# Optimization experiments

Hardware: AMD Instinct MI355X
Metric: run time of the kernel (lower is better)

## Reference

```python
import jax, jax.numpy as jnp
import numpy as np
from jax import lax

B, N, S, NSAMPLE = 8, 4096, 1024, 32
RADIUS = 0.2
EPS = 1e-5
IN_CH = 64
MLP = [64, 64, 128]


def _fps(xyz, npoint):
    # farthest point sampling; deterministic start at index 0 (torch uses a random start)
    b, n, _ = xyz.shape
    bidx = jnp.arange(b)

    def step(carry, _):
        distance, farthest = carry
        centroid = xyz[bidx, farthest][:, None, :]            # [B,1,3]
        d = jnp.sum((xyz - centroid) ** 2, axis=-1)           # [B,N]
        distance = jnp.minimum(distance, d)
        nxt = jnp.argmax(distance, axis=-1).astype(jnp.int32)
        return (distance, nxt), farthest

    init = (jnp.full((b, n), 1e10, dtype=xyz.dtype), jnp.zeros((b,), jnp.int32))
    _, idxs = lax.scan(step, init, None, length=npoint)
    return idxs.T                                             # [B,npoint]


def _index_points(p, idx):
    # p: [B,N,C], idx: [B,...] -> [B,...,C]
    return jax.vmap(lambda pp, ii: pp[ii])(p, idx)


def _square_distance(src, dst):
    # src [B,S,3], dst [B,N,3] -> [B,S,N]
    d = -2.0 * jnp.einsum('bsc,bnc->bsn', src, dst)
    d += jnp.sum(src ** 2, -1)[:, :, None]
    d += jnp.sum(dst ** 2, -1)[:, None, :]
    return d


def _query_ball(radius, nsample, xyz, new_xyz):
    n = xyz.shape[1]
    sqr = _square_distance(new_xyz, xyz)                      # [B,S,N]
    gidx = jnp.where(sqr > radius ** 2, n, jnp.arange(n, dtype=jnp.int32))
    gidx = jnp.sort(gidx, axis=-1)[:, :, :nsample]            # [B,S,nsample]
    first = gidx[:, :, :1]
    return jnp.where(gidx == n, first, gidx)


def setup_inputs() -> dict:
    key = jax.random.key(0)
    ks = jax.random.split(key, 8)
    inp = {
        'xyz': jax.random.uniform(ks[0], (B, N, 3), jnp.float32),
        'points': jax.random.normal(ks[1], (B, N, IN_CH), jnp.float32),
    }
    last = IN_CH + 3
    for i, out_c in enumerate(MLP):
        scale = 1.0 / np.sqrt(last)
        inp[f'w{i}'] = jax.random.normal(ks[2 + i], (out_c, last), jnp.float32) * scale
        inp[f'b{i}'] = jnp.zeros((out_c,), jnp.float32)
        inp[f'g{i}'] = jnp.ones((out_c,), jnp.float32)
        inp[f'be{i}'] = jnp.zeros((out_c,), jnp.float32)
        last = out_c
    return inp


def _forward(xyz, points, params):
    fps_idx = _fps(xyz, S)
    new_xyz = _index_points(xyz, fps_idx)                     # [B,S,3]
    idx = _query_ball(RADIUS, NSAMPLE, xyz, new_xyz)          # [B,S,n]
    grouped_xyz = _index_points(xyz, idx) - new_xyz[:, :, None, :]
    h = jnp.concatenate([grouped_xyz, _index_points(points, idx)], axis=-1)  # [B,S,n,67]
    for (w, b, g, be) in params:
        h = jnp.einsum('bsnc,oc->bsno', h, w) + b             # 1x1 conv
        mu = jnp.mean(h, axis=(0, 1, 2))
        var = jnp.var(h, axis=(0, 1, 2))                      # training-mode batch norm
        h = jax.nn.relu((h - mu) * lax.rsqrt(var + EPS) * g + be)
    new_points = jnp.max(h, axis=2)                           # [B,S,Cout]
    return new_xyz, jnp.transpose(new_points, (0, 2, 1))      # [B,Cout,S] like torch


def reference(xyz, points, w0, b0, g0, be0, w1, b1, g1, be1, w2, b2, g2, be2):
    params = [(w0, b0, g0, be0), (w1, b1, g1, be1), (w2, b2, g2, be2)]
    return _forward(xyz, points, params)
```

## Files before the change

### kernel.cpp

```cpp
#include <hip/hip_runtime.h>
#include <stdint.h>

#define NB 8
#define NPTS 4096
#define NS 1024
#define NK 32
#define NROWS (NB*NS*NK)
#define R2 0.04f
#define NCOPY 8

typedef __attribute__((ext_vector_type(8))) short bf16x8;
typedef __attribute__((ext_vector_type(4))) float f32x4;

__device__ __forceinline__ float bf2f(uint16_t u){
    uint32_t v = ((uint32_t)u) << 16;
    return __uint_as_float(v);
}
__device__ __forceinline__ uint16_t f2bf(float f){
    uint32_t u = __float_as_uint(f);
    uint32_t r = (u + 0x7FFFu + ((u >> 16) & 1u)) >> 16;
    return (uint16_t)r;
}
__device__ __forceinline__ bf16x8 load_bf8(const uint16_t* p){
    return *reinterpret_cast<const bf16x8*>(p);
}

#define DPPMAX64(key, ctrl, rmask)                                             \
    {                                                                          \
        uint32_t _lo = (uint32_t)(key), _hi = (uint32_t)((key) >> 32);         \
        uint32_t _olo = (uint32_t)__builtin_amdgcn_update_dpp(                 \
            0, (int)_lo, (ctrl), (rmask), 0xf, true);                          \
        uint32_t _ohi = (uint32_t)__builtin_amdgcn_update_dpp(                 \
            0, (int)_hi, (ctrl), (rmask), 0xf, true);                          \
        unsigned long long _o = (((unsigned long long)_ohi) << 32) | _olo;     \
        key = (_o > (key)) ? _o : (key);                                       \
    }

#define FT 16
__global__ __launch_bounds__(256) void fps_kernel(const float* __restrict__ xyz,
                                                  float* __restrict__ out_newxyz){
    __shared__ float LX[NPTS], LY[NPTS], LZ[NPTS];
    __shared__ float4 SC[NS];
    __shared__ unsigned long long cand[2][4];
    const int b = blockIdx.x, t = threadIdx.x;
    const float* base = xyz + (size_t)b * (NPTS*3);
    float px[FT], py[FT], pz[FT], pd[FT];
#pragma unroll
    for (int j = 0; j < FT; ++j){
        int i = t*FT + j;
        float x = base[i*3+0], y = base[i*3+1], z = base[i*3+2];
        px[j]=x; py[j]=y; pz[j]=z; pd[j]=1e10f;
        LX[i]=x; LY[i]=y; LZ[i]=z;
    }
    __syncthreads();
    int cur = 0;
    const int wave = t >> 6, lane = t & 63;
    for (int s = 0; s < NS; ++s){
        float cx = LX[cur], cy = LY[cur], cz = LZ[cur];
        if (t == 0) SC[s] = make_float4(cx, cy, cz, 0.f);
        float bestd = -1.0f; int besti = 0;
#pragma unroll
        for (int j = 0; j < FT; ++j){
            float d;
            {
#pragma clang fp contract(off)
                float dx = px[j]-cx, dy = py[j]-cy, dz = pz[j]-cz;
                d = ((dx*dx) + (dy*dy)) + (dz*dz);
            }
            float nd = fminf(pd[j], d);
            pd[j] = nd;
            if (nd > bestd){ bestd = nd; besti = t*FT + j; }
        }
        unsigned long long key =
            (((unsigned long long)__float_as_uint(bestd)) << 32) |
            (unsigned long long)(~(unsigned)besti);
        DPPMAX64(key, 0x111, 0xf);
        DPPMAX64(key, 0x112, 0xf);
        DPPMAX64(key, 0x114, 0xf);
        DPPMAX64(key, 0x118, 0xf);
        DPPMAX64(key, 0x142, 0xa);
        DPPMAX64(key, 0x143, 0xc);
        int p = s & 1;
        if (lane == 63) cand[p][wave] = key;
        __syncthreads();
        unsigned long long k0 = cand[p][0], k1 = cand[p][1];
        unsigned long long k2 = cand[p][2], k3 = cand[p][3];
        unsigned long long m01 = (k0 > k1) ? k0 : k1;
        unsigned long long m23 = (k2 > k3) ? k2 : k3;
        unsigned long long km  = (m01 > m23) ? m01 : m23;
        cur = (int)(~(uint32_t)km);
    }
    __syncthreads();
    for (int i = t; i < NS; i += 256){
        float4 c = SC[i];
        float* o = out_newxyz + ((size_t)b*NS + i)*3;
        o[0] = c.x; o[1] = c.y; o[2] = c.z;
    }
}

__global__ __launch_bounds__(256) void qball_kernel(const float* __restrict__ xyz,
                                                    const float* __restrict__ newxyz,
                                                    int* __restrict__ idx_out){
    int gid = blockIdx.x*256 + threadIdx.x;
    int w = gid >> 6, lane = gid & 63;
    int b = w >> 10;
    const float* q = newxyz + (size_t)w*3;
    float qx = q[0], qy = q[1], qz = q[2];
    float qn = qx*qx;
    qn = fmaf(qy, qy, qn);
    qn = fmaf(qz, qz, qn);
    const float* base = xyz + (size_t)b * (NPTS*3);
    int cnt = 0, first = 0;
    for (int c0 = 0; c0 < NPTS; c0 += 64){
        int i = c0 + lane;
        float x = base[i*3+0], y = base[i*3+1], z = base[i*3+2];
        float xn = x*x;
        xn = fmaf(y, y, xn);
        xn = fmaf(z, z, xn);
        float dot = qx*x;
        dot = fmaf(qy, y, dot);
        dot = fmaf(qz, z, dot);
        float d;
        {
#pragma clang fp contract(off)
            d = -2.0f * dot;
            d = d + qn;
            d = d + xn;
        }
        bool in = !(d > R2);
        unsigned long long m = __ballot(in);
        if (in){
            int rank = __popcll(m & ((1ull << lane) - 1ull));
            int pos = cnt + rank;
            if (pos < NK) idx_out[(size_t)w*NK + pos] = i;
        }
        if (cnt == 0 && m) first = c0 + (__ffsll((unsigned long long)m) - 1);
        cnt += __popcll(m);
        if (cnt >= NK) break;
    }
    if (cnt < NK){
        for (int p = cnt + lane; p < NK; p += 64) idx_out[(size_t)w*NK + p] = first;
    }
}

__global__ void prep_kernel(const float* __restrict__ w0, const float* __restrict__ w1,
                            const float* __restrict__ w2, uint16_t* __restrict__ w0b,
                            uint16_t* __restrict__ w1b, uint16_t* __restrict__ w2b){
    int t = blockIdx.x*256 + threadIdx.x;
    int stride = gridDim.x*256;
    for (int i = t; i < 64*96; i += stride){
        int n = i/96, c = i%96;
        w0b[i] = (c < 67) ? f2bf(w0[n*67 + c]) : (uint16_t)0;
    }
    for (int i = t; i < 64*64; i += stride)  w1b[i] = f2bf(w1[i]);
    for (int i = t; i < 128*64; i += stride) w2b[i] = f2bf(w2[i]);
}

__global__ __launch_bounds__(256) void layer0_mfma(const float* __restrict__ xyz,
                                                   const float* __restrict__ pts,
                                                   const int* __restrict__ idx,
                                                   const float* __restrict__ newxyz,
                                                   const uint16_t* __restrict__ w0b,
                                                   const float* __restrict__ b0,
                                                   uint16_t* __restrict__ z0,
                                                   double* __restrict__ accumOut){
    __shared__ float S_s[16][64], S_q[16][64];
    const int wave = threadIdx.x >> 6, lane = threadIdx.x & 63;
    const int q = lane >> 4, l16 = lane & 15;
    const int r0 = blockIdx.x*64 + wave*16;
    const int row = r0 + l16;
    const int b = row >> 15;
    const int bs = row >> 5;
    const int id = idx[row];
    const float* prow = pts + (((size_t)b << 12) + id)*64;
    const float* xr   = xyz + (((size_t)b << 12) + id)*3;
    const float* qr   = newxyz + (size_t)bs*3;
    float d0 = xr[0]-qr[0], d1 = xr[1]-qr[1], d2 = xr[2]-qr[2];

    bf16x8 Bf[4][3];
#pragma unroll
    for (int nt = 0; nt < 4; ++nt)
#pragma unroll
        for (int s = 0; s < 3; ++s)
            Bf[nt][s] = load_bf8(w0b + (nt*16 + l16)*96 + s*32 + q*8);

    f32x4 acc[4];
#pragma unroll
    for (int nt = 0; nt < 4; ++nt) acc[nt] = (f32x4){0.f,0.f,0.f,0.f};

#pragma unroll
    for (int s = 0; s < 3; ++s){
        const int k0 = s*32 + q*8;
        bf16x8 a;
#pragma unroll
        for (int j = 0; j < 8; ++j){
            int k = k0 + j;
            float v = (k < 3) ? ((k == 0) ? d0 : ((k == 1) ? d1 : d2))
                              : ((k < 67) ? prow[k-3] : 0.f);
            a[j] = (short)f2bf(v);
        }
#pragma unroll
        for (int nt = 0; nt < 4; ++nt)
            acc[nt] = __builtin_amdgcn_mfma_f32_16x16x32_bf16(a, Bf[nt][s], acc[nt], 0, 0, 0);
    }
#pragma unroll
    for (int nt = 0; nt < 4; ++nt){
        int c = nt*16 + l16;
        float bb = b0[c];
        float sps = 0.f, spq = 0.f;
#pragma unroll
        for (int reg = 0; reg < 4; ++reg){
            int rr = r0 + q*4 + reg;
            float h = acc[nt][reg] + bb;
            sps += h;
            spq = fmaf(h, h, spq);
            z0[(size_t)rr*64 + c] = f2bf(h);
        }
        S_s[wave*4 + q][c] = sps;
        S_q[wave*4 + q][c] = spq;
    }
    __syncthreads();
    int t = threadIdx.x;
    if (t < 64){
        double ss = 0.0, sq = 0.0;
#pragma unroll
        for (int i = 0; i < 16; ++i){ ss += (double)S_s[i][t]; sq += (double)S_q[i][t]; }
        int cp = blockIdx.x & (NCOPY-1);
        atomicAdd(&accumOut[cp*256 + t], ss);
        atomicAdd(&accumOut[cp*256 + 128 + t], sq);
    }
}

template<int COUT>
__global__ __launch_bounds__(256) void layer_mfma(const uint16_t* __restrict__ zin,
                                                  const double* __restrict__ accumIn,
                                                  const float* __restrict__ g,
                                                  const float* __restrict__ be,
                                                  const uint16_t* __restrict__ wb,
                                                  const float* __restrict__ bias,
                                                  uint16_t* __restrict__ zout,
                                                  double* __restrict__ accumOut){
    constexpr int NT = COUT/16;
    __shared__ float sc_l[64], sh_l[64];
    __shared__ float S_s[16][COUT], S_q[16][COUT];
    const int t = threadIdx.x;
    if (t < 64){
        double s = 0.0, qq = 0.0;
#pragma unroll
        for (int cp = 0; cp < NCOPY; ++cp){
            s  += accumIn[cp*256 + t];
            qq += accumIn[cp*256 + 128 + t];
        }
        double mean = s / (double)NROWS;
        double var  = qq / (double)NROWS - mean*mean;
        double rs = 1.0 / sqrt(var + 1e-5);
        double scv = (double)g[t] * rs;
        sc_l[t] = (float)scv;
        sh_l[t] = (float)((double)be[t] - mean*scv);
    }
    __syncthreads();

    const int wave = t >> 6, lane = t & 63;
    const int q = lane >> 4, l16 = lane & 15;
    const int r0 = blockIdx.x*64 + wave*16;

    bf16x8 Bf[NT][2];
#pragma unroll
    for (int nt = 0; nt < NT; ++nt)
#pragma unroll
        for (int s = 0; s < 2; ++s)
            Bf[nt][s] = load_bf8(wb + (nt*16 + l16)*64 + s*32 + q*8);

    float sc[2][8], sh[2][8];
#pragma unroll
    for (int s = 0; s < 2; ++s){
        float4 a0 = *reinterpret_cast<const float4*>(&sc_l[s*32 + q*8]);
        float4 a1 = *reinterpret_cast<const float4*>(&sc_l[s*32 + q*8 + 4]);
        float4 b0_ = *reinterpret_cast<const float4*>(&sh_l[s*32 + q*8]);
        float4 b1_ = *reinterpret_cast<const float4*>(&sh_l[s*32 + q*8 + 4]);
        sc[s][0]=a0.x; sc[s][1]=a0.y; sc[s][2]=a0.z; sc[s][3]=a0.w;
        sc[s][4]=a1.x; sc[s][5]=a1.y; sc[s][6]=a1.z; sc[s][7]=a1.w;
        sh[s][0]=b0_.x; sh[s][1]=b0_.y; sh[s][2]=b0_.z; sh[s][3]=b0_.w;
        sh[s][4]=b1_.x; sh[s][5]=b1_.y; sh[s][6]=b1_.z; sh[s][7]=b1_.w;
    }

    f32x4 acc[NT];
#pragma unroll
    for (int nt = 0; nt < NT; ++nt) acc[nt] = (f32x4){0.f,0.f,0.f,0.f};

    const uint16_t* zr = zin + (size_t)(r0 + l16)*64;
#pragma unroll
    for (int s = 0; s < 2; ++s){
        uint4 u = *reinterpret_cast<const uint4*>(zr + s*32 + q*8);
        float h[8];
        h[0] = bf2f((uint16_t)(u.x & 0xFFFF)); h[1] = bf2f((uint16_t)(u.x >> 16));
        h[2] = bf2f((uint16_t)(u.y & 0xFFFF)); h[3] = bf2f((uint16_t)(u.y >> 16));
        h[4] = bf2f((uint16_t)(u.z & 0xFFFF)); h[5] = bf2f((uint16_t)(u.z >> 16));
        h[6] = bf2f((uint16_t)(u.w & 0xFFFF)); h[7] = bf2f((uint16_t)(u.w >> 16));
        bf16x8 a;
#pragma unroll
        for (int j = 0; j < 8; ++j){
            float v = fmaxf(fmaf(h[j], sc[s][j], sh[s][j]), 0.f);
            a[j] = (short)f2bf(v);
        }
#pragma unroll
        for (int nt = 0; nt < NT; ++nt)
            acc[nt] = __builtin_amdgcn_mfma_f32_16x16x32_bf16(a, Bf[nt][s], acc[nt], 0, 0, 0);
    }
#pragma unroll
    for (int nt = 0; nt < NT; ++nt){
        int c = nt*16 + l16;
        float bb = bias[c];
        float sps = 0.f, spq = 0.f;
#pragma unroll
        for (int reg = 0; reg < 4; ++reg){
            int rr = r0 + q*4 + reg;
            float h = acc[nt][reg] + bb;
            sps += h;
            spq = fmaf(h, h, spq);
            zout[(size_t)rr*COUT + c] = f2bf(h);
        }
        S_s[wave*4 + q][c] = sps;
        S_q[wave*4 + q][c] = spq;
    }
    __syncthreads();
    if (t < COUT){
        double ss = 0.0, sq = 0.0;
#pragma unroll
        for (int i = 0; i < 16; ++i){ ss += (double)S_s[i][t]; sq += (double)S_q[i][t]; }
        int cp = blockIdx.x & (NCOPY-1);
        atomicAdd(&accumOut[cp*256 + t], ss);
        atomicAdd(&accumOut[cp*256 + 128 + t], sq);
    }
}

__global__ __launch_bounds__(256) void final_kernel(const uint16_t* __restrict__ z2,
                                                    const double* __restrict__ accumIn,
                                                    const float* __restrict__ g,
                                                    const float* __restrict__ be,
                                                    float* __restrict__ out){
    __shared__ float sc_l[128], sh_l[128];
    const int t0 = threadIdx.x;
    if (t0 < 128){
        double s = 0.0, qq = 0.0;
#pragma unroll
        for (int cp = 0; cp < NCOPY; ++cp){
            s  += accumIn[cp*256 + t0];
            qq += accumIn[cp*256 + 128 + t0];
        }
        double mean = s / (double)NROWS;
        double var  = qq / (double)NROWS - mean*mean;
        double rs = 1.0 / sqrt(var + 1e-5);
        double scv = (double)g[t0] * rs;
        sc_l[t0] = (float)scv;
        sh_l[t0] = (float)((double)be[t0] - mean*scv);
    }
    __syncthreads();

    int t = blockIdx.x*256 + threadIdx.x;
    int o = t & 127;
    int s = (t >> 7) & 1023;
    int b = t >> 17;
    const uint16_t* zr = z2 + ((size_t)(((b << 10) | s)) * NK) * 128 + o;
    float vmax = -1e30f, vmin = 1e30f;
#pragma unroll 4
    for (int k = 0; k < NK; ++k){
        float v = bf2f(zr[(size_t)k*128]);
        vmax = fmaxf(vmax, v);
        vmin = fminf(vmin, v);
    }
    float sc = sc_l[o], sh = sh_l[o];
    float zsel = (sc >= 0.f) ? vmax : vmin;
    float y = fmaxf(fmaf(zsel, sc, sh), 0.f);
    out[24576 + ((size_t)b << 17) + ((size_t)o << 10) + s] = y;
}

extern "C" void kernel_launch(void* const* d_in, const int* in_sizes, int n_in,
                              void* d_out, int out_size, void* d_ws, size_t ws_size,
                              hipStream_t stream) {
    const float* xyz = (const float*)d_in[0];
    const float* pts = (const float*)d_in[1];
    const float* w0  = (const float*)d_in[2];
    const float* b0  = (const float*)d_in[3];
    const float* g0  = (const float*)d_in[4];
    const float* be0 = (const float*)d_in[5];
    const float* w1  = (const float*)d_in[6];
    const float* b1  = (const float*)d_in[7];
    const float* g1  = (const float*)d_in[8];
    const float* be1 = (const float*)d_in[9];
    const float* w2  = (const float*)d_in[10];
    const float* b2  = (const float*)d_in[11];
    const float* g2  = (const float*)d_in[12];
    const float* be2 = (const float*)d_in[13];
    float* out = (float*)d_out;

    char* ws = (char*)d_ws;
    double*   accum0 = (double*)(ws + 0);
    double*   accum1 = (double*)(ws + 16384);
    double*   accum2 = (double*)(ws + 32768);
    uint16_t* w0b    = (uint16_t*)(ws + 49152);
    uint16_t* w1b    = (uint16_t*)(ws + 61440);
    uint16_t* w2b    = (uint16_t*)(ws + 69632);
    uint16_t* z0     = (uint16_t*)(ws + 86016);
    uint16_t* z1     = (uint16_t*)(ws + 33640448);
    uint16_t* z2     = (uint16_t*)(ws + 67194880);
    int*      idx    = (int*)(ws + 67194880);

    hipMemsetAsync(ws, 0, 49152, stream);

    prep_kernel<<<32, 256, 0, stream>>>(w0, w1, w2, w0b, w1b, w2b);
    fps_kernel<<<NB, 256, 0, stream>>>(xyz, out);
    qball_kernel<<<2048, 256, 0, stream>>>(xyz, out, idx);
    layer0_mfma<<<4096, 256, 0, stream>>>(xyz, pts, idx, out, w0b, b0, z0, accum0);
    layer_mfma<64><<<4096, 256, 0, stream>>>(z0, accum0, g0, be0, w1b, b1, z1, accum1);
    layer_mfma<128><<<4096, 256, 0, stream>>>(z1, accum1, g1, be1, w2b, b2, z2, accum2);
    final_kernel<<<4096, 256, 0, stream>>>(z2, accum2, g2, be2, out);
}
```

Before: 848.9 us.

## Fuse max/min pooling into layer-2 GEMM and drop the z2 round trip

```diff
diff --git a/kernel.cpp b/kernel.cpp
--- a/kernel.cpp
+++ b/kernel.cpp
@@ -7,7 +7,7 @@
 #define NK 32
 #define NROWS (NB*NS*NK)
 #define R2 0.04f
-#define NCOPY 8
+#define NCOPY 32
 
 typedef __attribute__((ext_vector_type(8))) short bf16x8;
 typedef __attribute__((ext_vector_type(4))) float f32x4;
@@ -39,9 +39,9 @@
 #define FT 16
 __global__ __launch_bounds__(256) void fps_kernel(const float* __restrict__ xyz,
                                                   float* __restrict__ out_newxyz){
-    __shared__ float LX[NPTS], LY[NPTS], LZ[NPTS];
+    __shared__ float4 LP[NPTS];
     __shared__ float4 SC[NS];
-    __shared__ unsigned long long cand[2][4];
+    __shared__ alignas(16) unsigned long long cand[2][4];
     const int b = blockIdx.x, t = threadIdx.x;
     const float* base = xyz + (size_t)b * (NPTS*3);
     float px[FT], py[FT], pz[FT], pd[FT];
@@ -50,13 +50,14 @@
         int i = t*FT + j;
         float x = base[i*3+0], y = base[i*3+1], z = base[i*3+2];
         px[j]=x; py[j]=y; pz[j]=z; pd[j]=1e10f;
-        LX[i]=x; LY[i]=y; LZ[i]=z;
+        LP[i] = make_float4(x, y, z, 0.f);
     }
     __syncthreads();
     int cur = 0;
     const int wave = t >> 6, lane = t & 63;
     for (int s = 0; s < NS; ++s){
-        float cx = LX[cur], cy = LY[cur], cz = LZ[cur];
+        float4 cp4 = LP[cur];
+        float cx = cp4.x, cy = cp4.y, cz = cp4.z;
         if (t == 0) SC[s] = make_float4(cx, cy, cz, 0.f);
         float bestd = -1.0f; int besti = 0;
 #pragma unroll
@@ -83,10 +84,10 @@
         int p = s & 1;
         if (lane == 63) cand[p][wave] = key;
         __syncthreads();
-        unsigned long long k0 = cand[p][0], k1 = cand[p][1];
-        unsigned long long k2 = cand[p][2], k3 = cand[p][3];
-        unsigned long long m01 = (k0 > k1) ? k0 : k1;
-        unsigned long long m23 = (k2 > k3) ? k2 : k3;
+        ulonglong2 c01 = *reinterpret_cast<const ulonglong2*>(&cand[p][0]);
+        ulonglong2 c23 = *reinterpret_cast<const ulonglong2*>(&cand[p][2]);
+        unsigned long long m01 = (c01.x > c01.y) ? c01.x : c01.y;
+        unsigned long long m23 = (c23.x > c23.y) ? c23.x : c23.y;
         unsigned long long km  = (m01 > m23) ? m01 : m23;
         cur = (int)(~(uint32_t)km);
     }
@@ -145,9 +146,11 @@
 
 __global__ void prep_kernel(const float* __restrict__ w0, const float* __restrict__ w1,
                             const float* __restrict__ w2, uint16_t* __restrict__ w0b,
-                            uint16_t* __restrict__ w1b, uint16_t* __restrict__ w2b){
+                            uint16_t* __restrict__ w1b, uint16_t* __restrict__ w2b,
+                            double* __restrict__ accumAll){
     int t = blockIdx.x*256 + threadIdx.x;
     int stride = gridDim.x*256;
+    for (int i = t; i < 3*NCOPY*256; i += stride) accumAll[i] = 0.0;
     for (int i = t; i < 64*96; i += stride){
         int n = i/96, c = i%96;
         w0b[i] = (c < 67) ? f2bf(w0[n*67 + c]) : (uint16_t)0;
@@ -231,18 +234,17 @@
     }
 }
 
-template<int COUT>
-__global__ __launch_bounds__(256) void layer_mfma(const uint16_t* __restrict__ zin,
-                                                  const double* __restrict__ accumIn,
-                                                  const float* __restrict__ g,
-                                                  const float* __restrict__ be,
-                                                  const uint16_t* __restrict__ wb,
-                                                  const float* __restrict__ bias,
-                                                  uint16_t* __restrict__ zout,
-                                                  double* __restrict__ accumOut){
-    constexpr int NT = COUT/16;
+__global__ __launch_bounds__(256) void layer1_mfma(const uint16_t* __restrict__ zin,
+                                                   const double* __restrict__ accumIn,
+                                                   const float* __restrict__ g,
+                                                   const float* __restrict__ be,
+                                                   const uint16_t* __restrict__ wb,
+                                                   const float* __restrict__ bias,
+                                                   uint16_t* __restrict__ zout,
+                                                   double* __restrict__ accumOut){
+    constexpr int NT = 4;
     __shared__ float sc_l[64], sh_l[64];
-    __shared__ float S_s[16][COUT], S_q[16][COUT];
+    __shared__ float S_s[16][64], S_q[16][64];
     const int t = threadIdx.x;
     if (t < 64){
         double s = 0.0, qq = 0.0;
@@ -273,16 +275,12 @@
 
     float sc[2][8], sh[2][8];
 #pragma unroll
-    for (int s = 0; s < 2; ++s){
-        float4 a0 = *reinterpret_cast<const float4*>(&sc_l[s*32 + q*8]);
-        float4 a1 = *reinterpret_cast<const float4*>(&sc_l[s*32 + q*8 + 4]);
-        float4 b0_ = *reinterpret_cast<const float4*>(&sh_l[s*32 + q*8]);
-        float4 b1_ = *reinterpret_cast<const float4*>(&sh_l[s*32 + q*8 + 4]);
-        sc[s][0]=a0.x; sc[s][1]=a0.y; sc[s][2]=a0.z; sc[s][3]=a0.w;
-        sc[s][4]=a1.x; sc[s][5]=a1.y; sc[s][6]=a1.z; sc[s][7]=a1.w;
-        sh[s][0]=b0_.x; sh[s][1]=b0_.y; sh[s][2]=b0_.z; sh[s][3]=b0_.w;
-        sh[s][4]=b1_.x; sh[s][5]=b1_.y; sh[s][6]=b1_.z; sh[s][7]=b1_.w;
-    }
+    for (int s = 0; s < 2; ++s)
+#pragma unroll
+        for (int j = 0; j < 8; ++j){
+            sc[s][j] = sc_l[s*32 + q*8 + j];
+            sh[s][j] = sh_l[s*32 + q*8 + j];
+        }
 
     f32x4 acc[NT];
 #pragma unroll
@@ -318,13 +316,13 @@
             float h = acc[nt][reg] + bb;
             sps += h;
             spq = fmaf(h, h, spq);
-            zout[(size_t)rr*COUT + c] = f2bf(h);
+            zout[(size_t)rr*64 + c] = f2bf(h);
         }
         S_s[wave*4 + q][c] = sps;
         S_q[wave*4 + q][c] = spq;
     }
     __syncthreads();
-    if (t < COUT){
+    if (t < 64){
         double ss = 0.0, sq = 0.0;
 #pragma unroll
         for (int i = 0; i < 16; ++i){ ss += (double)S_s[i][t]; sq += (double)S_q[i][t]; }
@@ -334,7 +332,120 @@
     }
 }
 
-__global__ __launch_bounds__(256) void final_kernel(const uint16_t* __restrict__ z2,
+__global__ __launch_bounds__(256) void layer2_mfma(const uint16_t* __restrict__ zin,
+                                                   const double* __restrict__ accumIn,
+                                                   const float* __restrict__ g,
+                                                   const float* __restrict__ be,
+                                                   const uint16_t* __restrict__ wb,
+                                                   const float* __restrict__ bias,
+                                                   float2* __restrict__ pool,
+                                                   double* __restrict__ accumOut){
+    constexpr int NT = 8;
+    __shared__ float sc_l[64], sh_l[64];
+    __shared__ float S_s[16][128], S_q[16][128];
+    __shared__ float P_mx[16][128], P_mn[16][128];
+    const int t = threadIdx.x;
+    if (t < 64){
+        double s = 0.0, qq = 0.0;
+#pragma unroll
+        for (int cp = 0; cp < NCOPY; ++cp){
+            s  += accumIn[cp*256 + t];
+            qq += accumIn[cp*256 + 128 + t];
+        }
+        double mean = s / (double)NROWS;
+        double var  = qq / (double)NROWS - mean*mean;
+        double rs = 1.0 / sqrt(var + 1e-5);
+        double scv = (double)g[t] * rs;
+        sc_l[t] = (float)scv;
+        sh_l[t] = (float)((double)be[t] - mean*scv);
+    }
+    __syncthreads();
+
+    const int wave = t >> 6, lane = t & 63;
+    const int q = lane >> 4, l16 = lane & 15;
+    const int r0 = blockIdx.x*64 + wave*16;
+
+    bf16x8 Bf[NT][2];
+#pragma unroll
+    for (int nt = 0; nt < NT; ++nt)
+#pragma unroll
+        for (int s = 0; s < 2; ++s)
+            Bf[nt][s] = load_bf8(wb + (nt*16 + l16)*64 + s*32 + q*8);
+
+    float sc[2][8], sh[2][8];
+#pragma unroll
+    for (int s = 0; s < 2; ++s)
+#pragma unroll
+        for (int j = 0; j < 8; ++j){
+            sc[s][j] = sc_l[s*32 + q*8 + j];
+            sh[s][j] = sh_l[s*32 + q*8 + j];
+        }
+
+    f32x4 acc[NT];
+#pragma unroll
+    for (int nt = 0; nt < NT; ++nt) acc[nt] = (f32x4){0.f,0.f,0.f,0.f};
+
+    const uint16_t* zr = zin + (size_t)(r0 + l16)*64;
+#pragma unroll
+    for (int s = 0; s < 2; ++s){
+        uint4 u = *reinterpret_cast<const uint4*>(zr + s*32 + q*8);
+        float h[8];
+        h[0] = bf2f((uint16_t)(u.x & 0xFFFF)); h[1] = bf2f((uint16_t)(u.x >> 16));
+        h[2] = bf2f((uint16_t)(u.y & 0xFFFF)); h[3] = bf2f((uint16_t)(u.y >> 16));
+        h[4] = bf2f((uint16_t)(u.z & 0xFFFF)); h[5] = bf2f((uint16_t)(u.z >> 16));
+        h[6] = bf2f((uint16_t)(u.w & 0xFFFF)); h[7] = bf2f((uint16_t)(u.w >> 16));
+        bf16x8 a;
+#pragma unroll
+        for (int j = 0; j < 8; ++j){
+            float v = fmaxf(fmaf(h[j], sc[s][j], sh[s][j]), 0.f);
+            a[j] = (short)f2bf(v);
+        }
+#pragma unroll
+        for (int nt = 0; nt < NT; ++nt)
+            acc[nt] = __builtin_amdgcn_mfma_f32_16x16x32_bf16(a, Bf[nt][s], acc[nt], 0, 0, 0);
+    }
+#pragma unroll
+    for (int nt = 0; nt < NT; ++nt){
+        int c = nt*16 + l16;
+        float bb = bias[c];
+        float sps = 0.f, spq = 0.f;
+        float mx = -1e30f, mn = 1e30f;
+#pragma unroll
+        for (int reg = 0; reg < 4; ++reg){
+            float h = acc[nt][reg] + bb;
+            sps += h;
+            spq = fmaf(h, h, spq);
+            mx = fmaxf(mx, h);
+            mn = fminf(mn, h);
+        }
+        S_s[wave*4 + q][c] = sps;
+        S_q[wave*4 + q][c] = spq;
+        P_mx[wave*4 + q][c] = mx;
+        P_mn[wave*4 + q][c] = mn;
+    }
+    __syncthreads();
+    if (t < 128){
+        double ss = 0.0, sq = 0.0;
+#pragma unroll
+        for (int i = 0; i < 16; ++i){ ss += (double)S_s[i][t]; sq += (double)S_q[i][t]; }
+        int cp = blockIdx.x & (NCOPY-1);
+        atomicAdd(&accumOut[cp*256 + t], ss);
+        atomicAdd(&accumOut[cp*256 + 128 + t], sq);
+    }
+    {
+        int gidx = t >> 7;
+        int c = t & 127;
+        float mx = -1e30f, mn = 1e30f;
+#pragma unroll
+        for (int i = 0; i < 8; ++i){
+            mx = fmaxf(mx, P_mx[gidx*8 + i][c]);
+            mn = fminf(mn, P_mn[gidx*8 + i][c]);
+        }
+        pool[(size_t)(blockIdx.x*2 + gidx)*128 + c] = make_float2(mx, mn);
+    }
+}
+
+__global__ __launch_bounds__(256) void final_kernel(const float2* __restrict__ pool,
                                                     const double* __restrict__ accumIn,
                                                     const float* __restrict__ g,
                                                     const float* __restrict__ be,
@@ -361,16 +472,9 @@
     int o = t & 127;
     int s = (t >> 7) & 1023;
     int b = t >> 17;
-    const uint16_t* zr = z2 + ((size_t)(((b << 10) | s)) * NK) * 128 + o;
-    float vmax = -1e30f, vmin = 1e30f;
-#pragma unroll 4
-    for (int k = 0; k < NK; ++k){
-        float v = bf2f(zr[(size_t)k*128]);
-        vmax = fmaxf(vmax, v);
-        vmin = fminf(vmin, v);
-    }
+    float2 p = pool[t];
     float sc = sc_l[o], sh = sh_l[o];
-    float zsel = (sc >= 0.f) ? vmax : vmin;
+    float zsel = (sc >= 0.f) ? p.x : p.y;
     float y = fmaxf(fmaf(zsel, sc, sh), 0.f);
     out[24576 + ((size_t)b << 17) + ((size_t)o << 10) + s] = y;
 }
@@ -396,23 +500,21 @@
 
     char* ws = (char*)d_ws;
     double*   accum0 = (double*)(ws + 0);
-    double*   accum1 = (double*)(ws + 16384);
-    double*   accum2 = (double*)(ws + 32768);
-    uint16_t* w0b    = (uint16_t*)(ws + 49152);
-    uint16_t* w1b    = (uint16_t*)(ws + 61440);
-    uint16_t* w2b    = (uint16_t*)(ws + 69632);
-    uint16_t* z0     = (uint16_t*)(ws + 86016);
-    uint16_t* z1     = (uint16_t*)(ws + 33640448);
-    uint16_t* z2     = (uint16_t*)(ws + 67194880);
-    int*      idx    = (int*)(ws + 67194880);
-
-    hipMemsetAsync(ws, 0, 49152, stream);
-
-    prep_kernel<<<32, 256, 0, stream>>>(w0, w1, w2, w0b, w1b, w2b);
+    double*   accum1 = (double*)(ws + 65536);
+    double*   accum2 = (double*)(ws + 131072);
+    uint16_t* w0b    = (uint16_t*)(ws + 196608);
+    uint16_t* w1b    = (uint16_t*)(ws + 208896);
+    uint16_t* w2b    = (uint16_t*)(ws + 217088);
+    uint16_t* z0     = (uint16_t*)(ws + 262144);
+    uint16_t* z1     = (uint16_t*)(ws + 33816576);
+    float2*   pool   = (float2*)  (ws + 67371008);
+    int*      idx    = (int*)     (ws + 75759616);
+
+    prep_kernel<<<32, 256, 0, stream>>>(w0, w1, w2, w0b, w1b, w2b, accum0);
     fps_kernel<<<NB, 256, 0, stream>>>(xyz, out);
     qball_kernel<<<2048, 256, 0, stream>>>(xyz, out, idx);
     layer0_mfma<<<4096, 256, 0, stream>>>(xyz, pts, idx, out, w0b, b0, z0, accum0);
-    layer_mfma<64><<<4096, 256, 0, stream>>>(z0, accum0, g0, be0, w1b, b1, z1, accum1);
-    layer_mfma<128><<<4096, 256, 0, stream>>>(z1, accum1, g1, be1, w2b, b2, z2, accum2);
-    final_kernel<<<4096, 256, 0, stream>>>(z2, accum2, g2, be2, out);
-}
+    layer1_mfma<<<4096, 256, 0, stream>>>(z0, accum0, g0, be0, w1b, b1, z1, accum1);
+    layer2_mfma<<<4096, 256, 0, stream>>>(z1, accum1, g1, be1, w2b, b2, pool, accum2);
+    final_kernel<<<4096, 256, 0, stream>>>(pool, accum2, g2, be2, out);
+}
```

Result: slower. 868.2 us (+2.3%).
